# Optimization experiments

Hardware: AMD Instinct MI355X
Metric: run time of the kernel (lower is better)

The kernel has to match this reference:

```python
import jax, jax.numpy as jnp
import numpy as np

BLOCK_SIZE = 16
E2M1_LOOKUP = jnp.array([0.0, 0.5, 1.0, 1.5, 2.0, 3.0, 4.0, 6.0], dtype=jnp.float32)


def setup_inputs() -> dict:
    key = jax.random.key(0)
    k1, k2, k3, k4, k5 = jax.random.split(key, 5)
    in_features, out_features = 8192, 8192
    x = jax.random.normal(k1, (64, in_features), dtype=jnp.float32)
    weight_packed = jax.random.randint(k2, (out_features, in_features // 2), 0, 256, dtype=jnp.int32)
    weight_scale = jax.random.uniform(k3, (out_features, in_features // BLOCK_SIZE), dtype=jnp.float32)
    weight_global_scale = jax.random.uniform(k4, (1,), dtype=jnp.float32) + 0.5
    bias = jax.random.normal(k5, (out_features,), dtype=jnp.float32)
    return {"x": x, "weight_packed": weight_packed, "weight_scale": weight_scale,
            "weight_global_scale": weight_global_scale, "bias": bias}


def unpack_nvfp4(weight_packed, weight_scale, weight_global_scale, dtype=jnp.float32):
    out_features, in_packed = weight_packed.shape
    in_features = in_packed * 2
    low = weight_packed & 15
    high = (weight_packed >> 4) & 15
    # per-byte order: low nibble first, then high nibble
    combined = jnp.stack([low, high], axis=-1).reshape(out_features, in_features)
    signs = (combined >> 3) & 1
    mag_idx = combined & 7
    values = E2M1_LOOKUP[mag_idx] * (1.0 - 2.0 * signs.astype(jnp.float32))
    # per-block (16-wide) scale
    values = (values.reshape(out_features, -1, BLOCK_SIZE) * weight_scale[..., None]).reshape(out_features, in_features)
    g = weight_global_scale.reshape(())
    actual_scale = jnp.where(g != 0, 1.0 / g, 1.0)
    return (values * actual_scale).astype(dtype)


def reference(x, weight_packed, weight_scale, weight_global_scale, bias):
    W = unpack_nvfp4(weight_packed, weight_scale, weight_global_scale, dtype=x.dtype)
    return x @ W.T + bias
```

## Files before the change

### kernel.cpp

```cpp
#include <hip/hip_runtime.h>
#include <stdint.h>

typedef _Float16 f16x2 __attribute__((ext_vector_type(2)));
typedef _Float16 f16x8 __attribute__((ext_vector_type(8)));
typedef float f32x4 __attribute__((ext_vector_type(4)));

static __device__ __forceinline__ uint32_t perm(uint32_t hi, uint32_t lo, uint32_t sel) {
    return __builtin_amdgcn_perm(hi, lo, sel);
}
static __device__ __forceinline__ f16x2 bch2(uint32_t u) { union { uint32_t x; f16x2 h; } c; c.x = u; return c.h; }
static __device__ __forceinline__ uint32_t bcu(f16x2 h) { union { uint32_t x; f16x2 h; } c; c.h = h; return c.x; }
static __device__ __forceinline__ uint32_t pkrtz(float a, float b) {
    auto r = __builtin_amdgcn_cvt_pkrtz(a, b);
    union { decltype(r) h; uint32_t u; } c; c.h = r; return c.u;
}

#define NTOT 8192
#define KTOT 8192
#define SPLITS 8
#define KCHUNK 1024
#define BN 128
#define PK 128
#define NPER (KCHUNK / PK)

__global__ __launch_bounds__(256, 2) void nvfp4_init_out(const float* __restrict__ bias,
                                                         float* __restrict__ out) {
    int i = blockIdx.x * 256 + threadIdx.x;
    ((f32x4*)out)[i] = ((const f32x4*)bias)[i & 2047];
}

__global__ __launch_bounds__(256, 2) void nvfp4_reduce(const float* __restrict__ part,
                                                       const float* __restrict__ bias,
                                                       float* __restrict__ out) {
    int i = blockIdx.x * 256 + threadIdx.x;
    f32x4 s = ((const f32x4*)bias)[i & 2047];
    #pragma unroll
    for (int p = 0; p < SPLITS; ++p) {
        f32x4 v = ((const f32x4*)part)[(size_t)p * 131072 + i];
        s = s + v;
    }
    ((f32x4*)out)[i] = s;
}

__global__ __launch_bounds__(512, 4) void nvfp4_gemm(const float* __restrict__ x,
                                                     const int* __restrict__ wp,
                                                     const float* __restrict__ wscale,
                                                     const float* __restrict__ gs,
                                                     float* __restrict__ dst,
                                                     int atomic_mode) {
    __shared__ uint32_t wl[2][128 * 16];
    __shared__ __align__(16) uint8_t xtl[2][64 * 256];
    __shared__ uint16_t scl[128 * 66];

    const int tid = threadIdx.x;
    const int nb = blockIdx.x & 63;
    const int ksp = blockIdx.x >> 6;
    const int nbase = nb * BN;
    const int kc0 = ksp * KCHUNK;

    const int lane = tid & 63;
    const int wid = tid >> 6;
    const int l15 = lane & 15;
    const int grp = lane >> 4;

    const int wsrow = tid >> 4;
    const int wss = tid & 15;
    const int* wgp = wp + (size_t)(nbase + wsrow) * 4096 + (kc0 >> 1) + wss * 4;
    const int xsrow = tid >> 3;
    const int xss = tid & 7;
    const float* xgp = x + (size_t)xsrow * KTOT + kc0 + xss * 4;

    int4 wst[4];
    f32x4 xst[4];

    auto issueW = [&](int p) {
        #pragma unroll
        for (int i = 0; i < 4; ++i)
            wst[i] = *(const int4*)(wgp + (size_t)i * 32 * 4096 + p * 64);
    };
    auto issueX = [&](int p) {
        #pragma unroll
        for (int j = 0; j < 4; ++j)
            xst[j] = *(const f32x4*)(xgp + p * 128 + j * 32);
    };
    auto writeW = [&](int p) {
        uint32_t* wb = wl[p & 1];
        #pragma unroll
        for (int i = 0; i < 4; ++i) {
            int R = wsrow + i * 32;
            uint32_t v = (uint32_t)(wst[i].x & 0xff) | ((uint32_t)(wst[i].y & 0xff) << 8) |
                         ((uint32_t)(wst[i].z & 0xff) << 16) | ((uint32_t)wst[i].w << 24);
            wb[R * 16 + (wss ^ (R & 15))] = v;
        }
    };
    auto writeX = [&](int p) {
        uint8_t* xb = xtl[p & 1];
        #pragma unroll
        for (int j = 0; j < 4; ++j) {
            uint32_t lo = pkrtz(xst[j].x, xst[j].y);
            uint32_t hi = pkrtz(xst[j].z, xst[j].w);
            int slot = j * 4 + (xss >> 1);
            uint32_t addr = (uint32_t)(xsrow * 256 + ((slot ^ (xsrow & 15)) << 4) + (xss & 1) * 8);
            uint2 dv; dv.x = lo; dv.y = hi;
            *(uint2*)(xb + addr) = dv;
        }
    };

    issueW(0);
    issueX(0);
    {
        float g = gs[0];
        float inv_g = (g != 0.0f) ? (1.0f / g) : 1.0f;
        int row = tid >> 2;
        int q = tid & 3;
        const float* sp = wscale + (size_t)(nbase + row) * 512 + (kc0 >> 4) + q * 16;
        #pragma unroll
        for (int j = 0; j < 4; ++j) {
            f32x4 v = *(const f32x4*)(sp + j * 4);
            uint32_t p01 = pkrtz(v.x * inv_g, v.y * inv_g);
            uint32_t p23 = pkrtz(v.z * inv_g, v.w * inv_g);
            uint32_t c = q * 16 + j * 4;
            *(uint32_t*)((uint8_t*)scl + row * 132 + c * 2) = p01;
            *(uint32_t*)((uint8_t*)scl + row * 132 + c * 2 + 4) = p23;
        }
    }
    writeW(0);
    writeX(0);
    __syncthreads();

    f32x4 acc[4];
    #pragma unroll
    for (int a = 0; a < 4; ++a)
        acc[a] = f32x4{0.f, 0.f, 0.f, 0.f};

    const uint32_t TH = 0x46444240u, TL = 0x3E3C3800u;
    const int srowb = (wid * 16 + l15) * 132;
    const int wR = wid * 16 + l15;

    for (int p = 0; p < NPER; ++p) {
        if (p + 1 < NPER) { issueW(p + 1); issueX(p + 1); }
        const uint32_t* wb = wl[p & 1];
        const uint8_t* xb = xtl[p & 1];

        #pragma unroll
        for (int tl = 0; tl < 4; ++tl) {
            f16x8 af[4];
            #pragma unroll
            for (int mt = 0; mt < 4; ++mt) {
                int row = mt * 16 + l15;
                uint32_t addr = (uint32_t)(row * 256 + (((tl * 4 + grp) ^ l15) << 4));
                af[mt] = *(const f16x8*)(xb + addr);
            }
            int scol = p * 8 + tl * 2 + (grp >> 1);
            uint32_t sr = *(const uint16_t*)((const uint8_t*)scl + srowb + scol * 2);
            f16x2 s2 = bch2(perm(0, sr, 0x01000100u));

            uint32_t b = wb[wR * 16 + ((tl * 4 + grp) ^ l15)];
            uint32_t sel_e = b & 0x07070707u;
            uint32_t sel_o = (b >> 4) & 0x07070707u;
            uint32_t he = perm(TH, TL, sel_e) | ((b & 0x08080808u) << 4);
            uint32_t ho = perm(TH, TL, sel_o) | (b & 0x80808080u);
            uint32_t d0 = perm(ho, he, 0x040C000Cu);
            uint32_t d1 = perm(ho, he, 0x050C010Cu);
            uint32_t d2 = perm(ho, he, 0x060C020Cu);
            uint32_t d3 = perm(ho, he, 0x070C030Cu);
            union { uint32_t u[4]; f16x8 h; } fr;
            fr.u[0] = bcu(bch2(d0) * s2);
            fr.u[1] = bcu(bch2(d1) * s2);
            fr.u[2] = bcu(bch2(d2) * s2);
            fr.u[3] = bcu(bch2(d3) * s2);
            #pragma unroll
            for (int mt = 0; mt < 4; ++mt)
                acc[mt] = __builtin_amdgcn_mfma_f32_16x16x32_f16(af[mt], fr.h, acc[mt], 0, 0, 0);
        }

        if (p + 1 < NPER) { writeW(p + 1); writeX(p + 1); }
        __syncthreads();
    }

    if (atomic_mode) {
        #pragma unroll
        for (int mt = 0; mt < 4; ++mt)
            #pragma unroll
            for (int q = 0; q < 4; ++q) {
                int row = mt * 16 + grp * 4 + q;
                int col = nbase + wid * 16 + l15;
                unsafeAtomicAdd(dst + (size_t)row * NTOT + col, acc[mt][q]);
            }
    } else {
        float* pd = dst + (size_t)ksp * 64 * NTOT;
        #pragma unroll
        for (int mt = 0; mt < 4; ++mt)
            #pragma unroll
            for (int q = 0; q < 4; ++q) {
                int row = mt * 16 + grp * 4 + q;
                int col = nbase + wid * 16 + l15;
                pd[(size_t)row * NTOT + col] = acc[mt][q];
            }
    }
}

extern "C" void kernel_launch(void* const* d_in, const int* in_sizes, int n_in,
                              void* d_out, int out_size, void* d_ws, size_t ws_size,
                              hipStream_t stream) {
    const float* x = (const float*)d_in[0];
    const int* wp = (const int*)d_in[1];
    const float* wscale = (const float*)d_in[2];
    const float* gs = (const float*)d_in[3];
    const float* bias = (const float*)d_in[4];
    float* out = (float*)d_out;

    const size_t need = (size_t)SPLITS * 64 * NTOT * sizeof(float);
    if (ws_size >= need) {
        nvfp4_gemm<<<dim3(SPLITS * (NTOT / BN)), dim3(512), 0, stream>>>(x, wp, wscale, gs, (float*)d_ws, 0);
        nvfp4_reduce<<<dim3(512), dim3(256), 0, stream>>>((const float*)d_ws, bias, out);
    } else {
        nvfp4_init_out<<<dim3(512), dim3(256), 0, stream>>>(bias, out);
        nvfp4_gemm<<<dim3(SPLITS * (NTOT / BN)), dim3(512), 0, stream>>>(x, wp, wscale, gs, out, 1);
    }
}
```

Before: 220.6 us.

## Prefetch global tiles two stages ahead with dual register buffers

Global loads for the weight and activation tiles are now issued two K-steps ahead into alternating register buffers (A/B), so more memory latency is hidden behind the MFMA work. The main loop is fully unrolled so the alternating buffer selection resolves at compile time. The __syncthreads calls are replaced with an inline s_waitcnt lgkmcnt(0) plus s_barrier, and the barrier after the last stage is skipped. This costs extra VGPRs for the second staging set, which under launch_bounds(512,4) could cause spills or lower occupancy.

```diff
diff --git a/kernel.cpp b/kernel.cpp
--- a/kernel.cpp
+++ b/kernel.cpp
@@ -70,20 +70,20 @@
     const int xss = tid & 7;
     const float* xgp = x + (size_t)xsrow * KTOT + kc0 + xss * 4;
 
-    int4 wst[4];
-    f32x4 xst[4];
-
-    auto issueW = [&](int p) {
+    int4 wstA[4], wstB[4];
+    f32x4 xstA[4], xstB[4];
+
+    auto issueW = [&](int p, int4* wst) {
         #pragma unroll
         for (int i = 0; i < 4; ++i)
             wst[i] = *(const int4*)(wgp + (size_t)i * 32 * 4096 + p * 64);
     };
-    auto issueX = [&](int p) {
+    auto issueX = [&](int p, f32x4* xst) {
         #pragma unroll
         for (int j = 0; j < 4; ++j)
             xst[j] = *(const f32x4*)(xgp + p * 128 + j * 32);
     };
-    auto writeW = [&](int p) {
+    auto writeW = [&](int p, const int4* wst) {
         uint32_t* wb = wl[p & 1];
         #pragma unroll
         for (int i = 0; i < 4; ++i) {
@@ -93,7 +93,7 @@
             wb[R * 16 + (wss ^ (R & 15))] = v;
         }
     };
-    auto writeX = [&](int p) {
+    auto writeX = [&](int p, const f32x4* xst) {
         uint8_t* xb = xtl[p & 1];
         #pragma unroll
         for (int j = 0; j < 4; ++j) {
@@ -106,27 +106,34 @@
         }
     };
 
-    issueW(0);
-    issueX(0);
+    issueW(0, wstA);
+    issueX(0, xstA);
+    const int srow_s = tid >> 2;
+    const int sq = tid & 3;
+    f32x4 sld[4];
+    {
+        const float* sp = wscale + (size_t)(nbase + srow_s) * 512 + (kc0 >> 4) + sq * 16;
+        #pragma unroll
+        for (int j = 0; j < 4; ++j)
+            sld[j] = *(const f32x4*)(sp + j * 4);
+    }
+    issueW(1, wstB);
+    issueX(1, xstB);
     {
         float g = gs[0];
         float inv_g = (g != 0.0f) ? (1.0f / g) : 1.0f;
-        int row = tid >> 2;
-        int q = tid & 3;
-        const float* sp = wscale + (size_t)(nbase + row) * 512 + (kc0 >> 4) + q * 16;
         #pragma unroll
         for (int j = 0; j < 4; ++j) {
-            f32x4 v = *(const f32x4*)(sp + j * 4);
-            uint32_t p01 = pkrtz(v.x * inv_g, v.y * inv_g);
-            uint32_t p23 = pkrtz(v.z * inv_g, v.w * inv_g);
-            uint32_t c = q * 16 + j * 4;
-            *(uint32_t*)((uint8_t*)scl + row * 132 + c * 2) = p01;
-            *(uint32_t*)((uint8_t*)scl + row * 132 + c * 2 + 4) = p23;
-        }
-    }
-    writeW(0);
-    writeX(0);
-    __syncthreads();
+            uint32_t p01 = pkrtz(sld[j].x * inv_g, sld[j].y * inv_g);
+            uint32_t p23 = pkrtz(sld[j].z * inv_g, sld[j].w * inv_g);
+            uint32_t c = sq * 16 + j * 4;
+            *(uint32_t*)((uint8_t*)scl + srow_s * 132 + c * 2) = p01;
+            *(uint32_t*)((uint8_t*)scl + srow_s * 132 + c * 2 + 4) = p23;
+        }
+    }
+    writeW(0, wstA);
+    writeX(0, xstA);
+    asm volatile("s_waitcnt lgkmcnt(0)\n\ts_barrier" ::: "memory");
 
     f32x4 acc[4];
     #pragma unroll
@@ -137,8 +144,12 @@
     const int srowb = (wid * 16 + l15) * 132;
     const int wR = wid * 16 + l15;
 
+    #pragma unroll
     for (int p = 0; p < NPER; ++p) {
-        if (p + 1 < NPER) { issueW(p + 1); issueX(p + 1); }
+        if (p + 2 < NPER) {
+            if ((p & 1) == 0) { issueW(p + 2, wstA); issueX(p + 2, xstA); }
+            else              { issueW(p + 2, wstB); issueX(p + 2, xstB); }
+        }
         const uint32_t* wb = wl[p & 1];
         const uint8_t* xb = xtl[p & 1];
 
@@ -174,8 +185,11 @@
                 acc[mt] = __builtin_amdgcn_mfma_f32_16x16x32_f16(af[mt], fr.h, acc[mt], 0, 0, 0);
         }
 
-        if (p + 1 < NPER) { writeW(p + 1); writeX(p + 1); }
-        __syncthreads();
+        if (p + 1 < NPER) {
+            if ((p & 1) == 0) { writeW(p + 1, wstB); writeX(p + 1, xstB); }
+            else              { writeW(p + 1, wstA); writeX(p + 1, xstA); }
+            asm volatile("s_waitcnt lgkmcnt(0)\n\ts_barrier" ::: "memory");
+        }
     }
 
     if (atomic_mode) {
```

After: 219.9 us. No clear change (-0.3%).
